# Performance work log

Hardware: AMD Instinct MI355X
Metric: run time of the kernel (lower is better)

## Reference

```python
import jax, jax.numpy as jnp
import numpy as np

K = 10                # knn neighbors
HEADS = 4             # attention heads
NAMES = ["self", "cross", "self", "cross", "self", "cross"]
SINKHORN_ITERS = 10


def _knn_graph_feature(x, k):
    # x: (b, c, n) -> (b, 2c, n, k), DGCNN-style graph feature
    xx = jnp.sum(x * x, axis=1)                              # (b, n)
    inner = jnp.einsum('bcn,bcm->bnm', x, x)
    dist = -xx[:, :, None] + 2.0 * inner - xx[:, None, :]    # negative squared L2
    idx = jax.lax.top_k(dist, k)[1]                          # (b, n, k)
    xt = jnp.transpose(x, (0, 2, 1))                         # (b, n, c)
    nbr = jax.vmap(lambda pts, id_: pts[id_])(xt, idx)       # (b, n, k, c)
    ctr = jnp.broadcast_to(xt[:, :, None, :], nbr.shape)
    feat = jnp.concatenate([nbr - ctr, ctr], axis=-1)        # (b, n, k, 2c)
    return jnp.transpose(feat, (0, 3, 1, 2))


def _encode(pts, w, b):
    # knn_feature: graph feature -> 1x1 conv2d -> mean over neighbors
    f = _knn_graph_feature(pts, K)                           # (b, 2c, n, k)
    y = jnp.einsum('oc,bcnk->bonk', w, f) + b[None, :, None, None]
    return y.mean(axis=-1)                                   # (b, d, n)


def _conv1(x, w, b):
    # 1x1 Conv1d
    return jnp.einsum('od,bdn->bon', w, x) + b[None, :, None]


def _bn(x, g, bt):
    # BatchNorm1d, training-mode batch statistics (biased var), eps=1e-5
    m = x.mean(axis=(0, 2), keepdims=True)
    v = ((x - m) ** 2).mean(axis=(0, 2), keepdims=True)
    return g[None, :, None] * (x - m) / jnp.sqrt(v + 1e-5) + bt[None, :, None]


def _mha(x, src, pw, pb, mw, mb):
    b, d, n = x.shape
    dim = d // HEADS
    q = _conv1(x, pw[0], pb[0]).reshape(b, dim, HEADS, -1)
    k = _conv1(src, pw[1], pb[1]).reshape(b, dim, HEADS, -1)
    v = _conv1(src, pw[2], pb[2]).reshape(b, dim, HEADS, -1)
    scores = jnp.einsum('bdhn,bdhm->bhnm', q, k) / (dim ** 0.5)
    prob = jax.nn.softmax(scores, axis=-1)
    out = jnp.einsum('bhnm,bdhm->bdhn', prob, v).reshape(b, d, -1)
    return _conv1(out, mw, mb)


def _prop(x, src, p):
    # AttentionalPropagation: MHA message + MLP([2d, 2d, d]) with BN+ReLU
    msg = _mha(x, src, p['pw'], p['pb'], p['mw'], p['mb'])
    y = jnp.concatenate([x, msg], axis=1)                    # (b, 2d, n)
    h = jax.nn.relu(_bn(_conv1(y, p['w1'], p['b1']), p['g'], p['bt']))
    return _conv1(h, p['w2'], p['b2'])


def _rodrigues(aa):
    # angle-axis (b,3) -> rotation matrices (b,3,3)
    theta = jnp.maximum(jnp.linalg.norm(aa, axis=-1, keepdims=True), 1e-8)
    r = aa / theta
    c = jnp.cos(theta)[..., None]
    s = jnp.sin(theta)[..., None]
    rx, ry, rz = r[..., 0], r[..., 1], r[..., 2]
    z = jnp.zeros_like(rx)
    Kmat = jnp.stack([jnp.stack([z, -rz, ry], -1),
                      jnp.stack([rz, z, -rx], -1),
                      jnp.stack([-ry, rx, z], -1)], -2)
    rrT = r[..., :, None] * r[..., None, :]
    I = jnp.eye(3, dtype=aa.dtype)
    return c * I + (1.0 - c) * rrT + s * Kmat


def reference(p2d, p3d, pose, enc2d_w, enc2d_b, enc3d_w, enc3d_b,
              proj_w, proj_b, merge_w, merge_b,
              mlp1_w, mlp1_b, bn_g, bn_b, mlp2_w, mlp2_b):
    # unit bearing vectors (assumption stated in weightedReprojectionErrorwithPose)
    f2 = p2d / jnp.linalg.norm(p2d, axis=-1, keepdims=True)
    desc0 = _encode(jnp.transpose(f2, (0, 2, 1)), enc2d_w, enc2d_b)   # (b, d, m)
    desc1 = _encode(jnp.transpose(p3d, (0, 2, 1)), enc3d_w, enc3d_b)  # (b, d, n)

    for i, name in enumerate(NAMES):
        p = dict(pw=proj_w[i], pb=proj_b[i], mw=merge_w[i], mb=merge_b[i],
                 w1=mlp1_w[i], b1=mlp1_b[i], g=bn_g[i], bt=bn_b[i],
                 w2=mlp2_w[i], b2=mlp2_b[i])
        s0, s1 = (desc1, desc0) if name == 'cross' else (desc0, desc1)
        d0 = desc0 + _prop(desc0, s0, p)
        d1 = desc1 + _prop(desc1, s1, p)
        desc0, desc1 = d0, d1

    # pairwiseL2Dist between descriptor sets
    f0 = jnp.transpose(desc0, (0, 2, 1))
    f1 = jnp.transpose(desc1, (0, 2, 1))
    n0 = jnp.sum(f0 * f0, -1)
    n1 = jnp.sum(f1 * f1, -1)
    dist2 = n0[:, :, None] + n1[:, None, :] - 2.0 * jnp.einsum('bmd,bnd->bmn', f0, f1)
    M = jnp.sqrt(jnp.clip(dist2, 1e-30, None))

    # log-space sinkhorn normalization -> joint weight matrix W
    log_alpha = -M
    for _ in range(SINKHORN_ITERS):
        log_alpha = log_alpha - jax.nn.logsumexp(log_alpha, axis=2, keepdims=True)
        log_alpha = log_alpha - jax.nn.logsumexp(log_alpha, axis=1, keepdims=True)
    W = jnp.exp(log_alpha)

    # weighted angular reprojection error at given pose (angle-axis + t)
    R = _rodrigues(pose[:, :3])
    t = pose[:, 3:]
    p3dt = jnp.einsum('bij,bnj->bni', R, p3d) + t[:, None, :]
    p3dt = p3dt / jnp.linalg.norm(p3dt, axis=-1, keepdims=True)
    err = jnp.einsum('bmn,bmn->b', W, 1.0 - jnp.einsum('bmd,bnd->bmn', f2, p3dt))
    return err


def setup_inputs() -> dict:
    key = jax.random.key(0)
    ks = jax.random.split(key, 12)
    B, Mpts, Npts, D, L = 4, 1024, 1024, 128, 6
    f = lambda k_, shp: jax.random.normal(k_, shp, dtype=jnp.float32) * 0.05
    return {
        'p2d': jax.random.normal(ks[0], (B, Mpts, 3), jnp.float32),
        'p3d': jax.random.normal(ks[1], (B, Npts, 3), jnp.float32),
        'pose': jax.random.normal(ks[2], (B, 6), jnp.float32) * 0.2,
        'enc2d_w': f(ks[3], (D, 6)), 'enc2d_b': jnp.zeros((D,), jnp.float32),
        'enc3d_w': f(ks[4], (D, 6)), 'enc3d_b': jnp.zeros((D,), jnp.float32),
        'proj_w': f(ks[5], (L, 3, D, D)), 'proj_b': jnp.zeros((L, 3, D), jnp.float32),
        'merge_w': f(ks[6], (L, D, D)), 'merge_b': jnp.zeros((L, D), jnp.float32),
        'mlp1_w': f(ks[7], (L, 2 * D, 2 * D)), 'mlp1_b': jnp.zeros((L, 2 * D), jnp.float32),
        'bn_g': jnp.ones((L, 2 * D), jnp.float32), 'bn_b': jnp.zeros((L, 2 * D), jnp.float32),
        'mlp2_w': f(ks[8], (L, D, 2 * D)), 'mlp2_b': jnp.zeros((L, D), jnp.float32),
    }
```

## Files before the change

kernel.cpp:

```cpp
#include <hip/hip_runtime.h>
#include <hip/hip_bf16.h>

constexpr int B   = 4;
constexpr int N   = 1024;
constexpr int D   = 128;
constexpr int KNN = 10;
constexpr int NH  = 4;

typedef _Float16 half2v __attribute__((ext_vector_type(2)));
typedef _Float16 f16x4  __attribute__((ext_vector_type(4)));
typedef _Float16 f16x8  __attribute__((ext_vector_type(8)));
typedef float    f32x4  __attribute__((ext_vector_type(4)));

static __device__ __forceinline__ half2v pkrtz(float a, float b) {
  return __builtin_bit_cast(half2v, __builtin_amdgcn_cvt_pkrtz(a, b));
}
static __device__ __forceinline__ float h2f(half2v h) {
  return __builtin_bit_cast(float, h);
}

__global__ __launch_bounds__(256) void k_norm2d(const float* __restrict__ p2d,
                                                float* __restrict__ f2) {
  int i = blockIdx.x * 256 + threadIdx.x;
  const float* p = p2d + (size_t)i * 3;
  float x = p[0], y = p[1], z = p[2];
  float inr = 1.f / sqrtf(x * x + y * y + z * z);
  float* o = f2 + (size_t)i * 3;
  o[0] = x * inr; o[1] = y * inr; o[2] = z * inr;
}

__global__ __launch_bounds__(256) void k_encode(const float* __restrict__ pts,
                                                const float* __restrict__ w,
                                                const float* __restrict__ bias,
                                                float* __restrict__ desc) {
  __shared__ float P[N][3];
  __shared__ float xx[N];
  __shared__ float dist[N];
  __shared__ float rv[256];
  __shared__ int   ri[256];
  __shared__ float feat[6];
  __shared__ int   nidx[KNN];
  int t = threadIdx.x;
  int n = blockIdx.x, b = blockIdx.y;
  const float* pb = pts + (size_t)b * N * 3;
  for (int i = t; i < N; i += 256) {
    float x = pb[i * 3 + 0], y = pb[i * 3 + 1], z = pb[i * 3 + 2];
    P[i][0] = x; P[i][1] = y; P[i][2] = z;
    xx[i] = x * x + y * y + z * z;
  }
  __syncthreads();
  float cx = P[n][0], cy = P[n][1], cz = P[n][2], cxx = xx[n];
  for (int i = t; i < N; i += 256) {
    float ip = cx * P[i][0] + cy * P[i][1] + cz * P[i][2];
    dist[i] = 2.f * ip - cxx - xx[i];
  }
  __syncthreads();
  for (int kk = 0; kk < KNN; ++kk) {
    float bv = -3.0e38f; int bi = N;
    for (int i = t; i < N; i += 256) {
      float v = dist[i];
      if (v > bv) { bv = v; bi = i; }
    }
    rv[t] = bv; ri[t] = bi;
    __syncthreads();
    for (int s = 128; s > 0; s >>= 1) {
      if (t < s) {
        float v2 = rv[t + s]; int i2 = ri[t + s];
        if (v2 > rv[t] || (v2 == rv[t] && i2 < ri[t])) { rv[t] = v2; ri[t] = i2; }
      }
      __syncthreads();
    }
    if (t == 0) { nidx[kk] = ri[0]; dist[ri[0]] = -3.0e38f; }
    __syncthreads();
  }
  if (t == 0) {
    float sx = 0, sy = 0, sz = 0;
    for (int kk = 0; kk < KNN; ++kk) {
      int i = nidx[kk];
      sx += P[i][0]; sy += P[i][1]; sz += P[i][2];
    }
    const float invk = 1.f / KNN;
    feat[0] = sx * invk - cx; feat[1] = sy * invk - cy; feat[2] = sz * invk - cz;
    feat[3] = cx; feat[4] = cy; feat[5] = cz;
  }
  __syncthreads();
  if (t < D) {
    const float* wr = w + t * 6;
    float a = bias[t];
#pragma unroll
    for (int j = 0; j < 6; ++j) a += wr[j] * feat[j];
    desc[((size_t)b * D + t) * N + n] = a;
  }
}

__global__ __launch_bounds__(256) void k_gemm(
    const float* __restrict__ pA0, const float* __restrict__ pA1,
    const float* __restrict__ pB0, const float* __restrict__ pB1,
    const float* __restrict__ w, const float* __restrict__ bias,
    const float* __restrict__ res, float* __restrict__ out,
    const float* __restrict__ stat, const float* __restrict__ g,
    const float* __restrict__ bt,
    int Cin, int catOff, size_t a_bstr, size_t b_bstr,
    int segCout, size_t segStride, int qkvMode) {
  __shared__ _Float16 As[64][48];
  __shared__ half2v   Bs[16][132];
  __shared__ float Ac[256], Bc[256];
  const int tid = threadIdx.x;
  const int wv  = tid >> 6;
  const int l   = tid & 63;
  const int wo  = wv >> 1;
  const int wn  = wv & 1;
  const int lr  = l & 15;
  const int lg  = l >> 4;
  const int o0 = blockIdx.y * 64;
  const int zb = blockIdx.x;
  const int z  = zb >> 3;
  const int n0 = (zb & 7) * 128;
  const int s = z >> 2, b = z & 3;
  const int seg = o0 / segCout;
  const int oo  = o0 % segCout;

  const float* XA = (s ? pA1 : pA0) + (size_t)b * a_bstr;
  const float* XB = pB0 ? ((s ? pB1 : pB0) + (size_t)b * b_bstr) : nullptr;
  const bool segB = qkvMode && (seg > 0);

  if (stat) {
    const float* st = stat + (size_t)s * 256 * 2;
    float A = st[tid * 2 + 1] * g[tid];
    Ac[tid] = A;
    Bc[tid] = fmaf(-st[tid * 2 + 0], A, bt[tid]);
  }

  f32x4 acc[2][4];
#pragma unroll
  for (int i = 0; i < 2; ++i)
#pragma unroll
    for (int j = 0; j < 4; ++j) acc[i][j] = (f32x4){0.f, 0.f, 0.f, 0.f};

  for (int kb = 0; kb < Cin; kb += 32) {
    __syncthreads();
#pragma unroll
    for (int j = 0; j < 2; ++j) {
      int idx = j * 256 + tid;
      int o = idx >> 3, c4 = (idx & 7) * 4;
      float4 wvv = *(const float4*)&w[(size_t)(o0 + o) * Cin + kb + c4];
      *(half2v*)&As[o][c4]     = pkrtz(wvv.x, wvv.y);
      *(half2v*)&As[o][c4 + 2] = pkrtz(wvv.z, wvv.w);
    }
#pragma unroll
    for (int j = 0; j < 2; ++j) {
      int idx = j * 256 + tid;
      int rp = idx >> 5, c4 = (idx & 31) * 4;
      int c0 = kb + 2 * rp, c1 = c0 + 1;
      const float* s0; int cc0 = c0;
      const float* s1; int cc1 = c1;
      if (qkvMode) {
        s0 = segB ? XB : XA; s1 = s0;
      } else {
        if (c0 >= catOff) { s0 = XB; cc0 = c0 - catOff; } else s0 = XA;
        if (c1 >= catOff) { s1 = XB; cc1 = c1 - catOff; } else s1 = XA;
      }
      float4 v0 = *(const float4*)&s0[(size_t)cc0 * N + n0 + c4];
      float4 v1 = *(const float4*)&s1[(size_t)cc1 * N + n0 + c4];
      if (stat) {
        float A0 = Ac[c0], B0 = Bc[c0], A1 = Ac[c1], B1 = Bc[c1];
        v0.x = fmaxf(fmaf(v0.x, A0, B0), 0.f);
        v0.y = fmaxf(fmaf(v0.y, A0, B0), 0.f);
        v0.z = fmaxf(fmaf(v0.z, A0, B0), 0.f);
        v0.w = fmaxf(fmaf(v0.w, A0, B0), 0.f);
        v1.x = fmaxf(fmaf(v1.x, A1, B1), 0.f);
        v1.y = fmaxf(fmaf(v1.y, A1, B1), 0.f);
        v1.z = fmaxf(fmaf(v1.z, A1, B1), 0.f);
        v1.w = fmaxf(fmaf(v1.w, A1, B1), 0.f);
      }
      float4 packed;
      packed.x = h2f(pkrtz(v0.x, v1.x));
      packed.y = h2f(pkrtz(v0.y, v1.y));
      packed.z = h2f(pkrtz(v0.z, v1.z));
      packed.w = h2f(pkrtz(v0.w, v1.w));
      *(float4*)&Bs[rp][c4] = packed;
    }
    __syncthreads();
    f16x8 afr0 = *(const f16x8*)&As[wo * 32 + lr][lg * 8];
    f16x8 afr1 = *(const f16x8*)&As[wo * 32 + 16 + lr][lg * 8];
#pragma unroll
    for (int tj = 0; tj < 4; ++tj) {
      int nn = wn * 64 + tj * 16 + lr;
      float4 btmp;
      btmp.x = *(const float*)&Bs[lg * 4 + 0][nn];
      btmp.y = *(const float*)&Bs[lg * 4 + 1][nn];
      btmp.z = *(const float*)&Bs[lg * 4 + 2][nn];
      btmp.w = *(const float*)&Bs[lg * 4 + 3][nn];
      f16x8 bfr = __builtin_bit_cast(f16x8, btmp);
      acc[0][tj] = __builtin_amdgcn_mfma_f32_16x16x32_f16(afr0, bfr, acc[0][tj], 0, 0, 0);
      acc[1][tj] = __builtin_amdgcn_mfma_f32_16x16x32_f16(afr1, bfr, acc[1][tj], 0, 0, 0);
    }
  }
#pragma unroll
  for (int ti = 0; ti < 2; ++ti) {
#pragma unroll
    for (int tj = 0; tj < 4; ++tj) {
      int nn = n0 + wn * 64 + tj * 16 + lr;
#pragma unroll
      for (int r = 0; r < 4; ++r) {
        int lrow = wo * 32 + ti * 16 + lg * 4 + r;
        size_t ob = (size_t)seg * segStride +
                    ((size_t)z * segCout + oo + lrow) * N + nn;
        float v = acc[ti][tj][r] + bias[o0 + lrow];
        if (res) v += res[ob];
        out[ob] = v;
      }
    }
  }
}

__global__ __launch_bounds__(512) void k_attn(const float* __restrict__ Q,
                                              const float* __restrict__ Kt,
                                              const float* __restrict__ Vt,
                                              float* __restrict__ O) {
  __shared__ _Float16 Klds[128][40];
  __shared__ _Float16 Vlds[32][136];
  const int t  = threadIdx.x;
  const int l  = t & 63, w = t >> 6;
  const int lr = l & 15, lg = l >> 4;
  const int q0 = blockIdx.x * 128 + w * 16;
  const int h  = blockIdx.y;
  const int z  = blockIdx.z;
  const size_t base = (size_t)z * (size_t)(D * N);
  const float* Kg = Kt + base + (size_t)h * N;
  const float* Vg = Vt + base + (size_t)h * N;
  const float scale = 0.17677669529663687f;

  f16x8 qfrag;
  {
    float qv[8];
#pragma unroll
    for (int j = 0; j < 8; ++j)
      qv[j] = Q[base + (size_t)((lg * 8 + j) * 4 + h) * N + q0 + lr] * scale;
    float4 qp;
    qp.x = h2f(pkrtz(qv[0], qv[1]));
    qp.y = h2f(pkrtz(qv[2], qv[3]));
    qp.z = h2f(pkrtz(qv[4], qv[5]));
    qp.w = h2f(pkrtz(qv[6], qv[7]));
    qfrag = __builtin_bit_cast(f16x8, qp);
  }

  f32x4 oacc0 = (f32x4){0.f, 0.f, 0.f, 0.f};
  f32x4 oacc1 = (f32x4){0.f, 0.f, 0.f, 0.f};
  float m = -1e30f, lsum = 0.f;

  for (int c = 0; c < 8; ++c) {
    const int k0 = c * 128;
    __syncthreads();
    {
      int kk = t & 127, d0 = (t >> 7) * 8;
      float kv[8];
#pragma unroll
      for (int j = 0; j < 8; ++j)
        kv[j] = Kg[(size_t)((d0 + j) * 4) * N + k0 + kk];
      float4 pk;
      pk.x = h2f(pkrtz(kv[0], kv[1]));
      pk.y = h2f(pkrtz(kv[2], kv[3]));
      pk.z = h2f(pkrtz(kv[4], kv[5]));
      pk.w = h2f(pkrtz(kv[6], kv[7]));
      *(float4*)&Klds[kk][d0] = pk;
      int dv = t & 31, ko = (t >> 5) * 8;
      const float* vp = Vg + (size_t)(dv * 4) * N + k0 + ko;
      float4 v0 = *(const float4*)vp;
      float4 v1 = *(const float4*)(vp + 4);
      float4 pv;
      pv.x = h2f(pkrtz(v0.x, v0.y)); pv.y = h2f(pkrtz(v0.z, v0.w));
      pv.z = h2f(pkrtz(v1.x, v1.y)); pv.w = h2f(pkrtz(v1.z, v1.w));
      *(float4*)&Vlds[dv][ko] = pv;
    }
    __syncthreads();
#pragma unroll
    for (int kt = 0; kt < 8; ++kt) {
      f16x8 kfrag = *(const f16x8*)&Klds[kt * 16 + lr][lg * 8];
      f32x4 s = __builtin_amdgcn_mfma_f32_16x16x32_f16(
          kfrag, qfrag, (f32x4){0.f, 0.f, 0.f, 0.f}, 0, 0, 0);
      float tmax = fmaxf(fmaxf(s[0], s[1]), fmaxf(s[2], s[3]));
      tmax = fmaxf(tmax, __shfl_xor(tmax, 16, 64));
      tmax = fmaxf(tmax, __shfl_xor(tmax, 32, 64));
      float nm = fmaxf(m, tmax);
      float corr = __expf(m - nm);
      m = nm;
      lsum *= corr;
#pragma unroll
      for (int r = 0; r < 4; ++r) { oacc0[r] *= corr; oacc1[r] *= corr; }
      float p0 = __expf(s[0] - m), p1 = __expf(s[1] - m);
      float p2 = __expf(s[2] - m), p3 = __expf(s[3] - m);
      float ts = p0 + p1 + p2 + p3;
      ts += __shfl_xor(ts, 16, 64);
      ts += __shfl_xor(ts, 32, 64);
      lsum += ts;
      float2 ptmp;
      ptmp.x = h2f(pkrtz(p0, p1));
      ptmp.y = h2f(pkrtz(p2, p3));
      f16x4 pfrag = __builtin_bit_cast(f16x4, ptmp);
      float2 vt0 = *(const float2*)&Vlds[lr][kt * 16 + lg * 4];
      float2 vt1 = *(const float2*)&Vlds[16 + lr][kt * 16 + lg * 4];
      f16x4 vf0 = __builtin_bit_cast(f16x4, vt0);
      f16x4 vf1 = __builtin_bit_cast(f16x4, vt1);
      oacc0 = __builtin_amdgcn_mfma_f32_16x16x16f16(vf0, pfrag, oacc0, 0, 0, 0);
      oacc1 = __builtin_amdgcn_mfma_f32_16x16x16f16(vf1, pfrag, oacc1, 0, 0, 0);
    }
  }
  float invL = 1.f / lsum;
#pragma unroll
  for (int r = 0; r < 4; ++r) {
    int d0 = lg * 4 + r;
    O[base + (size_t)(d0 * 4 + h) * N + q0 + lr] = oacc0[r] * invL;
    int d1 = 16 + lg * 4 + r;
    O[base + (size_t)(d1 * 4 + h) * N + q0 + lr] = oacc1[r] * invL;
  }
}

__global__ __launch_bounds__(256) void k_bnstat(const float* __restrict__ h,
                                                float* __restrict__ stat) {
  int c = blockIdx.x, s = blockIdx.y, t = threadIdx.x;
  __shared__ float red[256], red2[256];
  const float* base = h + ((size_t)s * B * 256 + c) * N;
  float sum = 0, sq = 0;
  for (int b = 0; b < B; ++b)
    for (int i = t; i < N; i += 256) {
      float v = base[(size_t)b * 256 * N + i];
      sum += v; sq = fmaf(v, v, sq);
    }
  red[t] = sum; red2[t] = sq; __syncthreads();
  for (int sft = 128; sft > 0; sft >>= 1) {
    if (t < sft) { red[t] += red[t + sft]; red2[t] += red2[t + sft]; }
    __syncthreads();
  }
  if (t == 0) {
    float mean = red[0] / (float)(B * N);
    float var = fmaxf(red2[0] / (float)(B * N) - mean * mean, 0.f);
    stat[(s * 256 + c) * 2 + 0] = mean;
    stat[(s * 256 + c) * 2 + 1] = 1.f / sqrtf(var + 1e-5f);
  }
}

__global__ __launch_bounds__(256) void k_dist(const float* __restrict__ d0,
                                              const float* __restrict__ d1,
                                              float* __restrict__ la) {
  __shared__ float xm[8][128];
  __shared__ float n0s[8];
  int m0 = blockIdx.x * 8, b = blockIdx.y, t = threadIdx.x;
  const float* p0 = d0 + (size_t)b * D * N;
  const float* p1 = d1 + (size_t)b * D * N;
  for (int i = t; i < 8 * 128; i += 256) {
    int mm = i >> 7, d = i & 127;
    xm[mm][d] = p0[(size_t)d * N + m0 + mm];
  }
  __syncthreads();
  if (t < 8) {
    float s = 0;
    for (int d = 0; d < 128; ++d) s += xm[t][d] * xm[t][d];
    n0s[t] = s;
  }
  __syncthreads();
  float dot[8][4] = {{0}};
  float n1[4] = {0, 0, 0, 0};
  for (int d = 0; d < 128; ++d) {
    float v[4];
#pragma unroll
    for (int u = 0; u < 4; ++u) {
      v[u] = p1[(size_t)d * N + t + u * 256];
      n1[u] = fmaf(v[u], v[u], n1[u]);
    }
#pragma unroll
    for (int mm = 0; mm < 8; ++mm) {
      float x = xm[mm][d];
#pragma unroll
      for (int u = 0; u < 4; ++u) dot[mm][u] = fmaf(x, v[u], dot[mm][u]);
    }
  }
  for (int mm = 0; mm < 8; ++mm) {
    float* row = la + ((size_t)b * N + m0 + mm) * N;
#pragma unroll
    for (int u = 0; u < 4; ++u) {
      float dist2 = fmaxf(n0s[mm] + n1[u] - 2.f * dot[mm][u], 1e-30f);
      row[t + u * 256] = -sqrtf(dist2);
    }
  }
}

__global__ __launch_bounds__(256) void k_row_r(const float* __restrict__ l0,
                                               const float* __restrict__ cvec,
                                               float* __restrict__ r,
                                               int useC) {
  __shared__ float red[256];
  int t = threadIdx.x;
  int bm = blockIdx.x;
  int b = bm >> 10;
  const float* row = l0 + (size_t)bm * N;
  float v0 = row[t], v1 = row[t + 256], v2 = row[t + 512], v3 = row[t + 768];
  if (useC) {
    const float* cl = cvec + (size_t)b * N;
    v0 -= cl[t]; v1 -= cl[t + 256]; v2 -= cl[t + 512]; v3 -= cl[t + 768];
  }
  float mx = fmaxf(fmaxf(v0, v1), fmaxf(v2, v3));
  red[t] = mx; __syncthreads();
  for (int s = 128; s > 0; s >>= 1) {
    if (t < s) red[t] = fmaxf(red[t], red[t + s]);
    __syncthreads();
  }
  mx = red[0]; __syncthreads();
  float se = __expf(v0 - mx) + __expf(v1 - mx) + __expf(v2 - mx) + __expf(v3 - mx);
  red[t] = se; __syncthreads();
  for (int s = 128; s > 0; s >>= 1) {
    if (t < s) red[t] += red[t + s];
    __syncthreads();
  }
  if (t == 0) r[bm] = mx + __logf(red[0]);
}

__global__ __launch_bounds__(256) void k_col_part(const float* __restrict__ l0,
                                                  const float* __restrict__ r,
                                                  float* __restrict__ pmax,
                                                  float* __restrict__ psum) {
  int t = threadIdx.x;
  int n = blockIdx.x * 256 + t;
  int p = blockIdx.y, b = blockIdx.z;
  const float* base = l0 + ((size_t)b * N + p * 32) * N + n;
  const float* rr = r + (size_t)b * N + p * 32;
  float mx = -1e30f, s = 0;
  for (int m = 0; m < 32; ++m) {
    float v = base[(size_t)m * N] - rr[m];
    if (v > mx) { s = s * __expf(mx - v) + 1.f; mx = v; }
    else s += __expf(v - mx);
  }
  pmax[((size_t)b * 32 + p) * N + n] = mx;
  psum[((size_t)b * 32 + p) * N + n] = s;
}

__global__ __launch_bounds__(256) void k_col_fin(const float* __restrict__ pmax,
                                                 const float* __restrict__ psum,
                                                 float* __restrict__ cvec) {
  int i = blockIdx.x * 256 + threadIdx.x;
  int b = i / N, n = i % N;
  float mx = -1e30f;
#pragma unroll
  for (int p = 0; p < 32; ++p) mx = fmaxf(mx, pmax[((size_t)b * 32 + p) * N + n]);
  float s = 0;
#pragma unroll
  for (int p = 0; p < 32; ++p)
    s += psum[((size_t)b * 32 + p) * N + n] * __expf(pmax[((size_t)b * 32 + p) * N + n] - mx);
  cvec[i] = mx + __logf(s);
}

__global__ __launch_bounds__(256) void k_rod(const float* __restrict__ pose,
                                             const float* __restrict__ p3d,
                                             float* __restrict__ p3dt) {
  int b = blockIdx.y;
  int n = blockIdx.x * 256 + threadIdx.x;
  const float* aa = pose + b * 6;
  float ax = aa[0], ay = aa[1], az = aa[2];
  float th = fmaxf(sqrtf(ax * ax + ay * ay + az * az), 1e-8f);
  float rx = ax / th, ry = ay / th, rz = az / th;
  float c = cosf(th), s = sinf(th), oc = 1.f - c;
  float R00 = c + oc * rx * rx,      R01 = oc * rx * ry - s * rz, R02 = oc * rx * rz + s * ry;
  float R10 = oc * ry * rx + s * rz, R11 = c + oc * ry * ry,      R12 = oc * ry * rz - s * rx;
  float R20 = oc * rz * rx - s * ry, R21 = oc * rz * ry + s * rx, R22 = c + oc * rz * rz;
  const float* p = p3d + ((size_t)b * N + n) * 3;
  float x = p[0], y = p[1], z = p[2];
  float X = R00 * x + R01 * y + R02 * z + aa[3];
  float Y = R10 * x + R11 * y + R12 * z + aa[4];
  float Z = R20 * x + R21 * y + R22 * z + aa[5];
  float inr = 1.f / sqrtf(X * X + Y * Y + Z * Z);
  float* o = p3dt + ((size_t)b * N + n) * 3;
  o[0] = X * inr; o[1] = Y * inr; o[2] = Z * inr;
}

__global__ __launch_bounds__(256) void k_err(const float* __restrict__ l0,
                                             const float* __restrict__ r,
                                             const float* __restrict__ cvec,
                                             const float* __restrict__ f2,
                                             const float* __restrict__ p3dt,
                                             float* __restrict__ rowsum) {
  __shared__ float red[256];
  int m = blockIdx.x, b = blockIdx.y, t = threadIdx.x;
  const float* row = l0 + ((size_t)b * N + m) * N;
  const float* cl = cvec + (size_t)b * N;
  const float rm = r[(size_t)b * N + m];
  const float* f = f2 + ((size_t)b * N + m) * 3;
  float fx = f[0], fy = f[1], fz = f[2];
  float s = 0;
  for (int n = t; n < N; n += 256) {
    const float* pp = p3dt + ((size_t)b * N + n) * 3;
    float dot = fx * pp[0] + fy * pp[1] + fz * pp[2];
    s += __expf(row[n] - rm - cl[n]) * (1.f - dot);
  }
  red[t] = s; __syncthreads();
  for (int sft = 128; sft > 0; sft >>= 1) {
    if (t < sft) red[t] += red[t + sft];
    __syncthreads();
  }
  if (t == 0) rowsum[(size_t)b * N + m] = red[0];
}

__global__ __launch_bounds__(256) void k_err_fin(const float* __restrict__ rowsum,
                                                 float* __restrict__ out) {
  __shared__ float red[256];
  int b = blockIdx.x, t = threadIdx.x;
  float s = 0;
  for (int i = t; i < N; i += 256) s += rowsum[(size_t)b * N + i];
  red[t] = s; __syncthreads();
  for (int sft = 128; sft > 0; sft >>= 1) {
    if (t < sft) red[t] += red[t + sft];
    __syncthreads();
  }
  if (t == 0) out[b] = red[0];
}

extern "C" void kernel_launch(void* const* d_in, const int* in_sizes, int n_in,
                              void* d_out, int out_size, void* d_ws, size_t ws_size,
                              hipStream_t stream) {
  const float* p2d     = (const float*)d_in[0];
  const float* p3d     = (const float*)d_in[1];
  const float* pose    = (const float*)d_in[2];
  const float* enc2d_w = (const float*)d_in[3];
  const float* enc2d_b = (const float*)d_in[4];
  const float* enc3d_w = (const float*)d_in[5];
  const float* enc3d_b = (const float*)d_in[6];
  const float* proj_w  = (const float*)d_in[7];
  const float* proj_b  = (const float*)d_in[8];
  const float* merge_w = (const float*)d_in[9];
  const float* merge_b = (const float*)d_in[10];
  const float* mlp1_w  = (const float*)d_in[11];
  const float* mlp1_b  = (const float*)d_in[12];
  const float* bn_g    = (const float*)d_in[13];
  const float* bn_b    = (const float*)d_in[14];
  const float* mlp2_w  = (const float*)d_in[15];
  const float* mlp2_b  = (const float*)d_in[16];

  float* W = (float*)d_ws;
  size_t off = 0;
  auto alloc = [&](size_t nelem) { float* p = W + off; off += nelem; return p; };
  const size_t SET = (size_t)B * D * N;
  float* f2    = alloc((size_t)B * N * 3);
  float* p3dt  = alloc((size_t)B * N * 3);
  float* descA = alloc(2 * SET);
  float* descB = alloc(2 * SET);
  float* qkv   = alloc(3 * 2 * SET);
  float* attnb = alloc(2 * SET);
  float* msgb  = alloc(2 * SET);
  float* hb    = alloc((size_t)2 * B * 256 * N);
  float* stat  = alloc(2 * 256 * 2);
  float* la    = alloc((size_t)B * N * N);
  float* pmax  = alloc((size_t)B * 32 * N);
  float* psum  = alloc((size_t)B * 32 * N);
  float* cvec  = alloc((size_t)B * N);
  float* rvec  = alloc((size_t)B * N);
  float* rowsum= alloc((size_t)B * N);
  (void)ws_size; (void)in_sizes; (void)n_in; (void)out_size;

  float* Qb = qkv;
  float* Kb = qkv + 2 * SET;
  float* Vb = qkv + 4 * SET;
  const size_t DS = (size_t)D * N;

  k_norm2d<<<(B * N) / 256, 256, 0, stream>>>(p2d, f2);
  k_encode<<<dim3(N, B), 256, 0, stream>>>(f2, enc2d_w, enc2d_b, descA);
  k_encode<<<dim3(N, B), 256, 0, stream>>>(p3d, enc3d_w, enc3d_b, descA + SET);

  float* dc = descA;
  float* dn = descB;
  for (int i = 0; i < 6; ++i) {
    int cross = (i & 1);
    const float* pw = proj_w + (size_t)i * 3 * D * D;
    const float* pb = proj_b + (size_t)i * 3 * D;
    float* d0 = dc;
    float* d1 = dc + SET;
    const float* sA = cross ? d1 : d0;
    const float* sB = cross ? d0 : d1;

    k_gemm<<<dim3(64, 6), 256, 0, stream>>>(
        d0, d1, sA, sB, pw, pb, nullptr, qkv, nullptr, nullptr, nullptr,
        D, D, DS, DS, D, 2 * SET, 1);
    k_attn<<<dim3(N / 128, NH, 2 * B), 512, 0, stream>>>(Qb, Kb, Vb, attnb);
    k_gemm<<<dim3(64, 2), 256, 0, stream>>>(
        attnb, attnb + SET, nullptr, nullptr, merge_w + (size_t)i * D * D,
        merge_b + (size_t)i * D, nullptr, msgb, nullptr, nullptr, nullptr,
        D, D, DS, DS, D, 0, 0);
    k_gemm<<<dim3(64, 4), 256, 0, stream>>>(
        dc, dc + SET, msgb, msgb + SET, mlp1_w + (size_t)i * 256 * 256,
        mlp1_b + (size_t)i * 256, nullptr, hb, nullptr, nullptr, nullptr,
        256, 128, DS, DS, 256, 0, 0);
    k_bnstat<<<dim3(256, 2), 256, 0, stream>>>(hb, stat);
    k_gemm<<<dim3(64, 2), 256, 0, stream>>>(
        hb, hb + (size_t)B * 256 * N, nullptr, nullptr,
        mlp2_w + (size_t)i * D * 256, mlp2_b + (size_t)i * D, dc, dn,
        stat, bn_g + (size_t)i * 256, bn_b + (size_t)i * 256,
        256, 256, (size_t)256 * N, 0, D, 0, 0);
    float* tmp = dc; dc = dn; dn = tmp;
  }

  k_dist<<<dim3(N / 8, B), 256, 0, stream>>>(dc, dc + SET, la);
  for (int it = 0; it < 10; ++it) {
    k_row_r<<<B * N, 256, 0, stream>>>(la, cvec, rvec, it > 0 ? 1 : 0);
    k_col_part<<<dim3(N / 256, 32, B), 256, 0, stream>>>(la, rvec, pmax, psum);
    k_col_fin<<<(B * N) / 256, 256, 0, stream>>>(pmax, psum, cvec);
  }
  k_rod<<<dim3(N / 256, B), 256, 0, stream>>>(pose, p3d, p3dt);
  k_err<<<dim3(N, B), 256, 0, stream>>>(la, rvec, cvec, f2, p3dt, rowsum);
  k_err_fin<<<B, 256, 0, stream>>>(rowsum, (float*)d_out);
}
```

Before: 938.3 us.

## Rewrite kNN encode to do one point per wavefront with register top-k

The encode kernel now assigns one query point to each 64-lane wavefront instead of one point per 256-thread block. Distances stay in registers, and each of the ten top-k rounds is a wavefront shuffle reduction, replacing the shared-memory tree reductions and their many block barriers. Each point cloud is loaded into shared memory once per four query points rather than once per point, and the grid shrinks by four. Point storage changes to struct-of-arrays to avoid bank conflicts. The cost is higher register pressure from the 16-entry distance array.

```diff
diff --git a/kernel.cpp b/kernel.cpp
--- a/kernel.cpp
+++ b/kernel.cpp
@@ -33,63 +33,60 @@
                                                 const float* __restrict__ w,
                                                 const float* __restrict__ bias,
                                                 float* __restrict__ desc) {
-  __shared__ float P[N][3];
-  __shared__ float xx[N];
-  __shared__ float dist[N];
-  __shared__ float rv[256];
-  __shared__ int   ri[256];
-  __shared__ float feat[6];
-  __shared__ int   nidx[KNN];
-  int t = threadIdx.x;
-  int n = blockIdx.x, b = blockIdx.y;
+  __shared__ float Px[N], Py[N], Pz[N], Xx[N];
+  const int t = threadIdx.x;
+  const int l = t & 63, wv = t >> 6;
+  const int n = blockIdx.x * 4 + wv;
+  const int b = blockIdx.y;
   const float* pb = pts + (size_t)b * N * 3;
   for (int i = t; i < N; i += 256) {
     float x = pb[i * 3 + 0], y = pb[i * 3 + 1], z = pb[i * 3 + 2];
-    P[i][0] = x; P[i][1] = y; P[i][2] = z;
-    xx[i] = x * x + y * y + z * z;
+    Px[i] = x; Py[i] = y; Pz[i] = z;
+    Xx[i] = x * x + y * y + z * z;
   }
   __syncthreads();
-  float cx = P[n][0], cy = P[n][1], cz = P[n][2], cxx = xx[n];
-  for (int i = t; i < N; i += 256) {
-    float ip = cx * P[i][0] + cy * P[i][1] + cz * P[i][2];
-    dist[i] = 2.f * ip - cxx - xx[i];
-  }
-  __syncthreads();
+  const float cx = Px[n], cy = Py[n], cz = Pz[n], cxx = Xx[n];
+  float dist[16];
+#pragma unroll
+  for (int i = 0; i < 16; ++i) {
+    int j = i * 64 + l;
+    float ip = cx * Px[j] + cy * Py[j] + cz * Pz[j];
+    dist[i] = 2.f * ip - cxx - Xx[j];
+  }
+  float sx = 0.f, sy = 0.f, sz = 0.f;
+#pragma unroll
   for (int kk = 0; kk < KNN; ++kk) {
-    float bv = -3.0e38f; int bi = N;
-    for (int i = t; i < N; i += 256) {
-      float v = dist[i];
-      if (v > bv) { bv = v; bi = i; }
-    }
-    rv[t] = bv; ri[t] = bi;
-    __syncthreads();
-    for (int s = 128; s > 0; s >>= 1) {
-      if (t < s) {
-        float v2 = rv[t + s]; int i2 = ri[t + s];
-        if (v2 > rv[t] || (v2 == rv[t] && i2 < ri[t])) { rv[t] = v2; ri[t] = i2; }
-      }
-      __syncthreads();
-    }
-    if (t == 0) { nidx[kk] = ri[0]; dist[ri[0]] = -3.0e38f; }
-    __syncthreads();
-  }
-  if (t == 0) {
-    float sx = 0, sy = 0, sz = 0;
-    for (int kk = 0; kk < KNN; ++kk) {
-      int i = nidx[kk];
-      sx += P[i][0]; sy += P[i][1]; sz += P[i][2];
-    }
-    const float invk = 1.f / KNN;
-    feat[0] = sx * invk - cx; feat[1] = sy * invk - cy; feat[2] = sz * invk - cz;
-    feat[3] = cx; feat[4] = cy; feat[5] = cz;
-  }
-  __syncthreads();
-  if (t < D) {
-    const float* wr = w + t * 6;
-    float a = bias[t];
+    float bv = dist[0]; int bi = l;
+#pragma unroll
+    for (int i = 1; i < 16; ++i) {
+      if (dist[i] > bv) { bv = dist[i]; bi = i * 64 + l; }
+    }
+#pragma unroll
+    for (int sft = 1; sft < 64; sft <<= 1) {
+      float v2 = __shfl_xor(bv, sft, 64);
+      int   i2 = __shfl_xor(bi, sft, 64);
+      if (v2 > bv || (v2 == bv && i2 < bi)) { bv = v2; bi = i2; }
+    }
+    sx += Px[bi]; sy += Py[bi]; sz += Pz[bi];
+    if ((bi & 63) == l) {
+      int io = bi >> 6;
+#pragma unroll
+      for (int i = 0; i < 16; ++i)
+        if (i == io) dist[i] = -3.0e38f;
+    }
+  }
+  const float invk = 1.f / KNN;
+  float feat[6];
+  feat[0] = sx * invk - cx; feat[1] = sy * invk - cy; feat[2] = sz * invk - cz;
+  feat[3] = cx; feat[4] = cy; feat[5] = cz;
+#pragma unroll
+  for (int rep = 0; rep < 2; ++rep) {
+    int c = rep * 64 + l;
+    const float* wr = w + c * 6;
+    float a = bias[c];
 #pragma unroll
     for (int j = 0; j < 6; ++j) a += wr[j] * feat[j];
-    desc[((size_t)b * D + t) * N + n] = a;
+    desc[((size_t)b * D + c) * N + n] = a;
   }
 }
 
@@ -561,8 +558,8 @@
   const size_t DS = (size_t)D * N;
 
   k_norm2d<<<(B * N) / 256, 256, 0, stream>>>(p2d, f2);
-  k_encode<<<dim3(N, B), 256, 0, stream>>>(f2, enc2d_w, enc2d_b, descA);
-  k_encode<<<dim3(N, B), 256, 0, stream>>>(p3d, enc3d_w, enc3d_b, descA + SET);
+  k_encode<<<dim3(N / 4, B), 256, 0, stream>>>(f2, enc2d_w, enc2d_b, descA);
+  k_encode<<<dim3(N / 4, B), 256, 0, stream>>>(p3d, enc3d_w, enc3d_b, descA + SET);
 
   float* dc = descA;
   float* dn = descB;
```

After: 874.7 us, median of 2. -6.8%, faster.
